# Kernel tuning notes

Measured on AMD Instinct MI355X. Metric: run time of the kernel, lower is better.

Reference implementation:

```python
import jax, jax.numpy as jnp
import numpy as np

V, E, SH, H = 10004, 300, 1024, 512
B, T = 128, 50
PAD = 10003


def setup_inputs() -> dict:
    key = jax.random.key(0)
    ks = jax.random.split(key, 13)
    s = 0.05
    emb = s * jax.random.normal(ks[0], (V, E), dtype=jnp.float32)
    emb = emb.at[PAD].set(0.0)  # padding_idx row is zero
    G = 2 * H  # GRU hidden size is 2*hid_size
    Wih = s * jax.random.normal(ks[1], (3 * G, E), dtype=jnp.float32)
    Whh = s * jax.random.normal(ks[2], (3 * G, G), dtype=jnp.float32)
    bih = s * jax.random.normal(ks[3], (3 * G,), dtype=jnp.float32)
    bhh = s * jax.random.normal(ks[4], (3 * G,), dtype=jnp.float32)
    W1 = s * jax.random.normal(ks[5], (H, SH), dtype=jnp.float32)
    b1 = s * jax.random.normal(ks[6], (H,), dtype=jnp.float32)
    W2 = s * jax.random.normal(ks[7], (E, G), dtype=jnp.float32)
    b2 = s * jax.random.normal(ks[8], (E,), dtype=jnp.float32)
    Wout = s * jax.random.normal(ks[9], (V, E), dtype=jnp.float32)
    ses_encoding = jax.random.normal(ks[10], (1, B, SH), dtype=jnp.float32)
    x = jax.random.randint(ks[11], (B, T), 0, 10000)
    return {"ses_encoding": ses_encoding, "x": x, "emb": emb, "Wih": Wih,
            "Whh": Whh, "bih": bih, "bhh": bhh, "W1": W1, "b1": b1,
            "W2": W2, "b2": b2, "Wout": Wout}


def reference(ses_encoding, x, emb, Wih, Whh, bih, bhh, W1, b1, W2, b2, Wout):
    hid = W1.shape[0]            # hid_size
    G = Whh.shape[1]             # 2*hid_size (GRU hidden)
    # ses_encoding = tanh(lin1(ses_encoding)), then viewed to [1, B, hid]
    ses = jnp.tanh(jnp.einsum('lbs,hs->lbh', ses_encoding, W1) + b1)[0]  # [B, hid]
    emb_all = emb[x]             # [B, T, E] (dropout inactive at eval)

    def step(h, e_t):
        # GRU hidden input each step: concat(prev_half, ses) -> [B, 2*hid]
        Hfull = jnp.concatenate([h, ses], axis=-1)
        gx = e_t @ Wih.T + bih                      # [B, 3G]
        gh = Hfull @ Whh.T + bhh                    # [B, 3G]
        r = jax.nn.sigmoid(gx[:, :G] + gh[:, :G])
        z = jax.nn.sigmoid(gx[:, G:2 * G] + gh[:, G:2 * G])
        n = jnp.tanh(gx[:, 2 * G:] + r * gh[:, 2 * G:])
        hnew = (1.0 - z) * n + z * Hfull            # [B, 2*hid]
        o = hnew @ W2.T + b2 + e_t                  # lin2(hid_o) + residual emb
        logits = o @ Wout.T                         # [B, V]
        return hnew[:, :hid], logits

    _, logits = jax.lax.scan(step, ses, jnp.swapaxes(emb_all, 0, 1))
    return jnp.swapaxes(logits, 0, 1)               # [B, T, V]
```

## Files before the change

kernel.cpp:

```cpp
#include <hip/hip_runtime.h>


typedef __bf16 bf16x8 __attribute__((ext_vector_type(8)));
typedef float f32x4 __attribute__((ext_vector_type(4)));
typedef unsigned long long u64;

struct CvtAll {
    const float* src[7];
    int srows[7], scols[7], sstride[7], soff[7], drows[7], dcols[7];
    __bf16* dst[7];
    int blk0[8];
    const int* x; const float* emb; __bf16* embbf;
};

__global__ void cvt_all_kernel(CvtAll p) {
    int bid = blockIdx.x;
    if (bid >= p.blk0[7]) {
        int idx = (bid - p.blk0[7]) * 256 + threadIdx.x;
        if (idx >= 6400 * 320) return;
        int m = idx / 320, c = idx - m * 320;
        int t = m >> 7, b = m & 127;
        int tok = p.x[b * 50 + t];
        float v = (c < 300) ? p.emb[(size_t)tok * 300 + c] : 0.0f;
        p.embbf[idx] = (__bf16)v;
        return;
    }
    int s = 0;
    while (s < 6 && bid >= p.blk0[s + 1]) ++s;
    int idx = (bid - p.blk0[s]) * 256 + threadIdx.x;
    int dc = p.dcols[s];
    int r = idx / dc, c = idx - r * dc;
    if (r >= p.drows[s]) return;
    float v = 0.0f;
    if (r < p.srows[s] && c < p.scols[s])
        v = p.src[s][(size_t)r * p.sstride[s] + p.soff[s] + c];
    p.dst[s][(size_t)r * dc + c] = (__bf16)v;
}

struct GemmParams {
    const __bf16* A; int lda;
    const __bf16* B; int ldb; int Brows;
    int K;
    const float* bias;
    float* outF; int ldo; int Nstore;
    __bf16* outBf;
    const __bf16* res;
    const float* add2;
    int ld2; int add2lim;
};

template <int EPI>
__launch_bounds__(256, 2)
__global__ void gemm_bt(GemmParams p) {
    __shared__ __bf16 As[128][40];
    __shared__ __bf16 Bs[128][40];

    const int tid = threadIdx.x;
    const int lane = tid & 63;
    const int wid = tid >> 6;
    const int wr = wid >> 1, wc = wid & 1;
    const int m0 = blockIdx.x * 128, c0 = blockIdx.y * 128;
    const int lrow = lane & 15;
    const int kq = lane >> 4;

    f32x4 acc[4][4];
#pragma unroll
    for (int i = 0; i < 4; ++i)
#pragma unroll
        for (int j = 0; j < 4; ++j) acc[i][j] = (f32x4){0.f, 0.f, 0.f, 0.f};

    for (int kb = 0; kb < p.K; kb += 32) {
#pragma unroll
        for (int i = 0; i < 2; ++i) {
            int chunk = i * 256 + tid;
            int row = chunk >> 2;
            int cc = (chunk & 3) * 8;
            bf16x8 va = *reinterpret_cast<const bf16x8*>(
                p.A + (size_t)(m0 + row) * p.lda + kb + cc);
            *reinterpret_cast<bf16x8*>(&As[row][cc]) = va;
            bf16x8 vb;
#pragma unroll
            for (int q = 0; q < 8; ++q) vb[q] = (__bf16)0.0f;
            int grow = c0 + row;
            if (grow < p.Brows)
                vb = *reinterpret_cast<const bf16x8*>(
                    p.B + (size_t)grow * p.ldb + kb + cc);
            *reinterpret_cast<bf16x8*>(&Bs[row][cc]) = vb;
        }
        __syncthreads();

        bf16x8 af[4], bfr[4];
#pragma unroll
        for (int m = 0; m < 4; ++m)
            af[m] = *reinterpret_cast<const bf16x8*>(&As[wr * 64 + m * 16 + lrow][kq * 8]);
#pragma unroll
        for (int n = 0; n < 4; ++n)
            bfr[n] = *reinterpret_cast<const bf16x8*>(&Bs[wc * 64 + n * 16 + lrow][kq * 8]);
#pragma unroll
        for (int m = 0; m < 4; ++m)
#pragma unroll
            for (int n = 0; n < 4; ++n)
                acc[m][n] = __builtin_amdgcn_mfma_f32_16x16x32_bf16(
                    af[m], bfr[n], acc[m][n], 0, 0, 0);
        __syncthreads();
    }

#pragma unroll
    for (int m = 0; m < 4; ++m) {
#pragma unroll
        for (int n = 0; n < 4; ++n) {
#pragma unroll
            for (int i = 0; i < 4; ++i) {
                int r = m0 + wr * 64 + m * 16 + kq * 4 + i;
                int c = c0 + wc * 64 + n * 16 + lrow;
                float v = acc[m][n][i];
                if constexpr (EPI == 1) {
                    v = tanhf(v + p.bias[c]);
                    p.outBf[(size_t)r * p.ldo + c] = (__bf16)v;
                    p.outF[(size_t)c * 128 + r] = v;
                } else if constexpr (EPI == 2) {
                    int ro = (r & 127) * 50 + (r >> 7);
                    if (c < 300) {
                        v += p.bias[c] + (float)p.res[(size_t)r * 320 + c];
                        p.outBf[(size_t)ro * 320 + c] = (__bf16)v;
                    } else if (c < 320) {
                        p.outBf[(size_t)ro * 320 + c] = (__bf16)0.0f;
                    }
                } else if constexpr (EPI == 3) {
                    if (c < p.Nstore) p.outF[(size_t)r * p.ldo + c] = v;
                } else {
                    if (c < p.Brows) {
                        float v2 = v + p.bias[r];
                        if (p.add2 && r < p.add2lim)
                            v2 += p.add2[(size_t)r * 128 + (c & 127)];
                        p.outF[(size_t)(c >> 7) * p.ldo + (size_t)r * 128 + (c & 127)] = v2;
                    }
                }
            }
        }
    }
}

#define SCAN_NB 64
__launch_bounds__(256, 1)
__global__ void scan_kernel(const __bf16* __restrict__ Whh_a,
                            const float* __restrict__ gxT,
                            const float* __restrict__ ghcT,
                            const float* __restrict__ sesT,
                            u64* __restrict__ F,
                            unsigned* __restrict__ cnt) {
    __shared__ char smem[131072];
    char* Ws = smem;
    char* Hs = smem + 98304;
    const int tid = threadIdx.x;
    const int lane = tid & 63;
    const int wid = tid >> 6;
    const int wr = wid >> 1, wc = wid & 1;
    const int bid = blockIdx.x;
    const int q = bid >> 4;
    const int j0 = (bid & 15) * 32;
    const int lrow = lane & 15, kq = lane >> 4;

    for (int it = 0; it < 24; ++it) {
        int c = it * 256 + tid;
        int rl = c >> 6, o16 = c & 63;
        int g = rl >> 5, jj = rl & 31;
        bf16x8 v = *reinterpret_cast<const bf16x8*>(
            Whh_a + (size_t)(g * 1024 + j0 + jj) * 512 + o16 * 8);
        *reinterpret_cast<bf16x8*>(Ws + rl * 1024 + ((o16 * 16) ^ ((rl & 7) << 4))) = v;
    }

    const int b_g = q * 32 + wc * 16 + lrow;
    const int jbase = j0 + wr * 16 + kq * 4;

    float cn[4], hprev[4], gcur[12], gpre[12];
#pragma unroll
    for (int i = 0; i < 4; ++i) {
        cn[i] = ghcT[(size_t)(2048 + jbase + i) * 128 + b_g];
        hprev[i] = sesT[(size_t)(jbase + i) * 128 + b_g];
    }
#pragma unroll
    for (int i = 0; i < 4; ++i) {
        gpre[i]     = gxT[(size_t)(jbase + i) * 128 + b_g];
        gpre[4 + i] = gxT[(size_t)(1024 + jbase + i) * 128 + b_g];
        gpre[8 + i] = gxT[(size_t)(2048 + jbase + i) * 128 + b_g];
    }

    for (int t = 0; t < 50; ++t) {
        for (int it = 0; it < 16; ++it) {
            int c = it * 256 + tid;
            int rl = c >> 7, o8 = c & 127;
            u64 v = __hip_atomic_load(
                F + ((size_t)t * 128 + q * 32 + rl) * 256 + o8,
                __ATOMIC_RELAXED, __HIP_MEMORY_SCOPE_AGENT);
            *reinterpret_cast<u64*>(Hs + rl * 1024 + ((o8 * 8) ^ ((rl & 7) << 4))) = v;
        }
#pragma unroll
        for (int i = 0; i < 12; ++i) gcur[i] = gpre[i];
        {
            int tn = (t < 49) ? t + 1 : 49;
            const float* gxt = gxT + (size_t)tn * 3072 * 128;
#pragma unroll
            for (int i = 0; i < 4; ++i) {
                gpre[i]     = gxt[(size_t)(jbase + i) * 128 + b_g];
                gpre[4 + i] = gxt[(size_t)(1024 + jbase + i) * 128 + b_g];
                gpre[8 + i] = gxt[(size_t)(2048 + jbase + i) * 128 + b_g];
            }
        }
        __syncthreads();

        f32x4 acc[3];
#pragma unroll
        for (int g = 0; g < 3; ++g) acc[g] = (f32x4){0.f, 0.f, 0.f, 0.f};
        const int hrow = wc * 16 + lrow;
        const int arow0 = wr * 16 + lrow;
        for (int kb = 0; kb < 16; ++kb) {
            int ko = kb * 64 + kq * 16;
            bf16x8 hfrag = *reinterpret_cast<const bf16x8*>(
                Hs + hrow * 1024 + (ko ^ ((hrow & 7) << 4)));
#pragma unroll
            for (int g = 0; g < 3; ++g) {
                int arow = g * 32 + arow0;
                bf16x8 wfrag = *reinterpret_cast<const bf16x8*>(
                    Ws + arow * 1024 + (ko ^ ((arow & 7) << 4)));
                acc[g] = __builtin_amdgcn_mfma_f32_16x16x32_bf16(
                    wfrag, hfrag, acc[g], 0, 0, 0);
            }
        }

        union { u64 u; __bf16 h[4]; } pk;
#pragma unroll
        for (int i = 0; i < 4; ++i) {
            float r = 1.0f / (1.0f + expf(-(gcur[i] + acc[0][i])));
            float z = 1.0f / (1.0f + expf(-(gcur[4 + i] + acc[1][i])));
            float nn = tanhf(gcur[8 + i] + r * (acc[2][i] + cn[i]));
            float hn = (1.0f - z) * nn + z * hprev[i];
            hprev[i] = hn;
            pk.h[i] = (__bf16)hn;
        }
        __hip_atomic_store(
            F + ((size_t)(t + 1) * 128 + b_g) * 256 + (jbase >> 2), pk.u,
            __ATOMIC_RELAXED, __HIP_MEMORY_SCOPE_AGENT);

        if (t < 49) {
            __syncthreads();
            if (tid == 0) {
                __hip_atomic_fetch_add(cnt + q * 32, 1u,
                                       __ATOMIC_RELAXED, __HIP_MEMORY_SCOPE_AGENT);
                unsigned tgt = (unsigned)(t + 1) * 16u;
                while (__hip_atomic_load(cnt + q * 32, __ATOMIC_RELAXED,
                                         __HIP_MEMORY_SCOPE_AGENT) < tgt)
                    __builtin_amdgcn_s_sleep(1);
            }
            __syncthreads();
        }
    }
}

__launch_bounds__(256, 1)
__global__ void tail_kernel(const __bf16* __restrict__ Whh_a,
                            const float* __restrict__ gxT,
                            const float* __restrict__ ghcT,
                            const float* __restrict__ sesT,
                            __bf16* __restrict__ F) {
    __shared__ char smem[131072];
    char* Ws = smem;
    char* Hs = smem + 98304;
    const int tid = threadIdx.x;
    const int lane = tid & 63;
    const int wid = tid >> 6;
    const int wr = wid >> 1, wc = wid & 1;
    const int bid = blockIdx.x;
    const int tseg = bid >> 6;
    const int rem = bid & 63;
    const int q = rem >> 4;
    const int j0 = 512 + (rem & 15) * 32;
    const int lrow = lane & 15, kq = lane >> 4;

    const int t0 = (tseg < 2) ? tseg * 13 : 26 + (tseg - 2) * 12;
    const int t1 = (tseg < 2) ? t0 + 13 : t0 + 12;

    for (int it = 0; it < 24; ++it) {
        int c = it * 256 + tid;
        int rl = c >> 6, o16 = c & 63;
        int g = rl >> 5, jj = rl & 31;
        bf16x8 v = *reinterpret_cast<const bf16x8*>(
            Whh_a + (size_t)(g * 1024 + j0 + jj) * 512 + o16 * 8);
        *reinterpret_cast<bf16x8*>(Ws + rl * 1024 + ((o16 * 16) ^ ((rl & 7) << 4))) = v;
    }

    const int b_g = q * 32 + wc * 16 + lrow;
    const int jbase = j0 + wr * 16 + kq * 4;

    float cn[4], sv[4];
#pragma unroll
    for (int i = 0; i < 4; ++i) {
        cn[i] = ghcT[(size_t)(2048 + jbase + i) * 128 + b_g];
        sv[i] = sesT[(size_t)(jbase + i - 512) * 128 + b_g];
    }

    for (int tt = t0; tt < t1; ++tt) {
        for (int it = 0; it < 8; ++it) {
            int c = it * 256 + tid;
            int rl = c >> 6, o16 = c & 63;
            bf16x8 v = *reinterpret_cast<const bf16x8*>(
                F + ((size_t)tt * 128 + q * 32 + rl) * 1024 + o16 * 8);
            *reinterpret_cast<bf16x8*>(Hs + rl * 1024 + ((o16 * 16) ^ ((rl & 7) << 4))) = v;
        }
        const float* gxt = gxT + (size_t)tt * 3072 * 128;
        float g0[12];
#pragma unroll
        for (int i = 0; i < 4; ++i) {
            g0[i]     = gxt[(size_t)(jbase + i) * 128 + b_g];
            g0[4 + i] = gxt[(size_t)(1024 + jbase + i) * 128 + b_g];
            g0[8 + i] = gxt[(size_t)(2048 + jbase + i) * 128 + b_g];
        }
        __syncthreads();

        f32x4 acc[3];
#pragma unroll
        for (int g = 0; g < 3; ++g) acc[g] = (f32x4){0.f, 0.f, 0.f, 0.f};
        const int hrow = wc * 16 + lrow;
        const int arow0 = wr * 16 + lrow;
        for (int kb = 0; kb < 16; ++kb) {
            int ko = kb * 64 + kq * 16;
            bf16x8 hfrag = *reinterpret_cast<const bf16x8*>(
                Hs + hrow * 1024 + (ko ^ ((hrow & 7) << 4)));
#pragma unroll
            for (int g = 0; g < 3; ++g) {
                int arow = g * 32 + arow0;
                bf16x8 wfrag = *reinterpret_cast<const bf16x8*>(
                    Ws + arow * 1024 + (ko ^ ((arow & 7) << 4)));
                acc[g] = __builtin_amdgcn_mfma_f32_16x16x32_bf16(
                    wfrag, hfrag, acc[g], 0, 0, 0);
            }
        }

        union { u64 u; __bf16 h[4]; } pk;
#pragma unroll
        for (int i = 0; i < 4; ++i) {
            float r = 1.0f / (1.0f + expf(-(g0[i] + acc[0][i])));
            float z = 1.0f / (1.0f + expf(-(g0[4 + i] + acc[1][i])));
            float nn = tanhf(g0[8 + i] + r * (acc[2][i] + cn[i]));
            pk.h[i] = (__bf16)((1.0f - z) * nn + z * sv[i]);
        }
        *reinterpret_cast<u64*>(F + ((size_t)(tt + 1) * 128 + b_g) * 1024 + jbase) = pk.u;
        __syncthreads();
    }
}

extern "C" void kernel_launch(void* const* d_in, const int* in_sizes, int n_in,
                              void* d_out, int out_size, void* d_ws, size_t ws_size,
                              hipStream_t stream) {
    const float* ses_enc = (const float*)d_in[0];
    const int*   x       = (const int*)d_in[1];
    const float* emb     = (const float*)d_in[2];
    const float* Wih     = (const float*)d_in[3];
    const float* Whh     = (const float*)d_in[4];
    const float* bih     = (const float*)d_in[5];
    const float* bhh     = (const float*)d_in[6];
    const float* W1      = (const float*)d_in[7];
    const float* b1      = (const float*)d_in[8];
    const float* W2      = (const float*)d_in[9];
    const float* b2      = (const float*)d_in[10];
    const float* Wout    = (const float*)d_in[11];
    float* out = (float*)d_out;

    char* ws = (char*)d_ws;
    float*  sesT      = (float*)(ws + 0);
    float*  ghcT      = (float*)(ws + 262144);
    __bf16* o_bf      = (__bf16*)(ws + 1835008);
    __bf16* W1_bf     = (__bf16*)(ws + 5931008);
    __bf16* Whh_a_bf  = (__bf16*)(ws + 6979584);
    __bf16* Whh_b_bf  = (__bf16*)(ws + 10125312);
    __bf16* Wih_bf    = (__bf16*)(ws + 13271040);
    __bf16* W2_bf     = (__bf16*)(ws + 15237120);
    __bf16* Wout_bf   = (__bf16*)(ws + 15851520);
    __bf16* sesenc_bf = (__bf16*)(ws + 22323200);
    unsigned* cnt     = (unsigned*)(ws + 22585344);

    char* ob = (char*)d_out;
    float*  gxT     = (float*)ob;
    __bf16* emb_bf  = (__bf16*)(ob + 80000000);
    __bf16* F       = (__bf16*)(ob + 88000000);

    dim3 blk(256);

    CvtAll ca;
    const float* csrc[7]  = {W1, Whh, Whh, Wih, W2, Wout, ses_enc};
    int csr[7]  = {512, 3072, 3072, 3072, 300, 10004, 128};
    int csc[7]  = {1024, 512, 512, 300, 1024, 300, 1024};
    int cst[7]  = {1024, 1024, 1024, 300, 1024, 300, 1024};
    int cso[7]  = {0, 0, 512, 0, 0, 0, 0};
    __bf16* cdst[7] = {W1_bf, Whh_a_bf, Whh_b_bf, Wih_bf, W2_bf, Wout_bf, sesenc_bf};
    int cdr[7]  = {512, 3072, 3072, 3072, 300, 10112, 128};
    int cdc[7]  = {1024, 512, 512, 320, 1024, 320, 1024};
    int b0 = 0;
    for (int s = 0; s < 7; ++s) {
        ca.src[s] = csrc[s]; ca.srows[s] = csr[s]; ca.scols[s] = csc[s];
        ca.sstride[s] = cst[s]; ca.soff[s] = cso[s];
        ca.dst[s] = cdst[s]; ca.drows[s] = cdr[s]; ca.dcols[s] = cdc[s];
        ca.blk0[s] = b0;
        b0 += (cdr[s] * cdc[s] + 255) / 256;
    }
    ca.blk0[7] = b0;
    ca.x = x; ca.emb = emb; ca.embbf = emb_bf;
    int total_blocks = b0 + (6400 * 320) / 256;
    cvt_all_kernel<<<total_blocks, 256, 0, stream>>>(ca);
    hipMemsetAsync(cnt, 0, 1024, stream);

    GemmParams P;

    P = {sesenc_bf, 1024, W1_bf, 1024, 512, 1024, b1, sesT, 1024, 512, F,
         nullptr, nullptr, 0, 0};
    gemm_bt<1><<<dim3(1, 4), blk, 0, stream>>>(P);

    P = {Whh_b_bf, 512, F, 1024, 128, 512, bhh, ghcT, 0, 0, nullptr,
         nullptr, nullptr, 0, 0};
    gemm_bt<4><<<dim3(24, 1), blk, 0, stream>>>(P);

    P = {Wih_bf, 320, emb_bf, 320, 6400, 320, bih, gxT, 3072 * 128, 0, nullptr,
         nullptr, ghcT, 0, 2048};
    gemm_bt<4><<<dim3(24, 50), blk, 0, stream>>>(P);

    scan_kernel<<<SCAN_NB, 256, 0, stream>>>(
        Whh_a_bf, gxT, ghcT, sesT, (u64*)F, cnt);

    tail_kernel<<<256, 256, 0, stream>>>(Whh_a_bf, gxT, ghcT, sesT, F);

    P = {F + 128 * 1024, 1024, W2_bf, 1024, 300, 1024, b2, nullptr, 0, 300, o_bf,
         emb_bf, nullptr, 0, 0};
    gemm_bt<2><<<dim3(50, 3), blk, 0, stream>>>(P);

    P = {o_bf, 320, Wout_bf, 320, 10112, 320, nullptr, out, 10004, 10004, nullptr,
         nullptr, nullptr, 0, 0};
    gemm_bt<3><<<dim3(50, 79), blk, 0, stream>>>(P);

    (void)in_sizes; (void)n_in; (void)out_size; (void)ws_size;
}
```

Before: 684.9 us.

## Prefetch next K tile into registers and widen GEMM K tile to 64

Restructures the bf16 MFMA GEMM main loop so that global loads for the next K block are issued into registers before the current block's MFMAs run. The staging into shared memory then happens at the top of the next iteration. The K tile doubles from 32 to 64, with shared arrays widened to match, which halves the number of barrier pairs per GEMM. This aims to hide global-memory latency behind compute, at the cost of more registers and LDS per block. It also assumes K is a multiple of 64.

```diff
diff --git a/kernel.cpp b/kernel.cpp
--- a/kernel.cpp
+++ b/kernel.cpp
@@ -52,8 +52,8 @@
 template <int EPI>
 __launch_bounds__(256, 2)
 __global__ void gemm_bt(GemmParams p) {
-    __shared__ __bf16 As[128][40];
-    __shared__ __bf16 Bs[128][40];
+    __shared__ __bf16 As[128][72];
+    __shared__ __bf16 Bs[128][72];
 
     const int tid = threadIdx.x;
     const int lane = tid & 63;
@@ -63,46 +63,79 @@
     const int lrow = lane & 15;
     const int kq = lane >> 4;
 
+    int srow[4], scol[4];
+#pragma unroll
+    for (int i = 0; i < 4; ++i) {
+        int chunk = i * 256 + tid;
+        srow[i] = chunk >> 3;
+        scol[i] = (chunk & 7) * 8;
+    }
+
     f32x4 acc[4][4];
 #pragma unroll
     for (int i = 0; i < 4; ++i)
 #pragma unroll
         for (int j = 0; j < 4; ++j) acc[i][j] = (f32x4){0.f, 0.f, 0.f, 0.f};
 
-    for (int kb = 0; kb < p.K; kb += 32) {
-#pragma unroll
-        for (int i = 0; i < 2; ++i) {
-            int chunk = i * 256 + tid;
-            int row = chunk >> 2;
-            int cc = (chunk & 3) * 8;
-            bf16x8 va = *reinterpret_cast<const bf16x8*>(
-                p.A + (size_t)(m0 + row) * p.lda + kb + cc);
-            *reinterpret_cast<bf16x8*>(&As[row][cc]) = va;
-            bf16x8 vb;
-#pragma unroll
-            for (int q = 0; q < 8; ++q) vb[q] = (__bf16)0.0f;
-            int grow = c0 + row;
-            if (grow < p.Brows)
-                vb = *reinterpret_cast<const bf16x8*>(
-                    p.B + (size_t)grow * p.ldb + kb + cc);
-            *reinterpret_cast<bf16x8*>(&Bs[row][cc]) = vb;
-        }
+    const int nkb = p.K >> 6;
+    bf16x8 ra[4], rb[4];
+#pragma unroll
+    for (int i = 0; i < 4; ++i) {
+        ra[i] = *reinterpret_cast<const bf16x8*>(
+            p.A + (size_t)(m0 + srow[i]) * p.lda + scol[i]);
+        bf16x8 z;
+#pragma unroll
+        for (int q = 0; q < 8; ++q) z[q] = (__bf16)0.0f;
+        int grow = c0 + srow[i];
+        rb[i] = (grow < p.Brows)
+            ? *reinterpret_cast<const bf16x8*>(p.B + (size_t)grow * p.ldb + scol[i])
+            : z;
+    }
+
+    for (int kb = 0; kb < nkb; ++kb) {
         __syncthreads();
-
-        bf16x8 af[4], bfr[4];
-#pragma unroll
-        for (int m = 0; m < 4; ++m)
-            af[m] = *reinterpret_cast<const bf16x8*>(&As[wr * 64 + m * 16 + lrow][kq * 8]);
-#pragma unroll
-        for (int n = 0; n < 4; ++n)
-            bfr[n] = *reinterpret_cast<const bf16x8*>(&Bs[wc * 64 + n * 16 + lrow][kq * 8]);
-#pragma unroll
-        for (int m = 0; m < 4; ++m)
+#pragma unroll
+        for (int i = 0; i < 4; ++i) {
+            *reinterpret_cast<bf16x8*>(&As[srow[i]][scol[i]]) = ra[i];
+            *reinterpret_cast<bf16x8*>(&Bs[srow[i]][scol[i]]) = rb[i];
+        }
+        __syncthreads();
+
+        if (kb + 1 < nkb) {
+            int ko = (kb + 1) << 6;
+#pragma unroll
+            for (int i = 0; i < 4; ++i) {
+                ra[i] = *reinterpret_cast<const bf16x8*>(
+                    p.A + (size_t)(m0 + srow[i]) * p.lda + ko + scol[i]);
+                bf16x8 z;
+#pragma unroll
+                for (int q = 0; q < 8; ++q) z[q] = (__bf16)0.0f;
+                int grow = c0 + srow[i];
+                rb[i] = (grow < p.Brows)
+                    ? *reinterpret_cast<const bf16x8*>(
+                          p.B + (size_t)grow * p.ldb + ko + scol[i])
+                    : z;
+            }
+        }
+
+#pragma unroll
+        for (int kk = 0; kk < 2; ++kk) {
+            bf16x8 af[4], bfr[4];
+#pragma unroll
+            for (int m = 0; m < 4; ++m)
+                af[m] = *reinterpret_cast<const bf16x8*>(
+                    &As[wr * 64 + m * 16 + lrow][kk * 32 + kq * 8]);
 #pragma unroll
             for (int n = 0; n < 4; ++n)
-                acc[m][n] = __builtin_amdgcn_mfma_f32_16x16x32_bf16(
-                    af[m], bfr[n], acc[m][n], 0, 0, 0);
-        __syncthreads();
+                bfr[n] = *reinterpret_cast<const bf16x8*>(
+                    &Bs[wc * 64 + n * 16 + lrow][kk * 32 + kq * 8]);
+#pragma unroll
+            for (int m = 0; m < 4; ++m)
+#pragma unroll
+                for (int n = 0; n < 4; ++n)
+                    acc[m][n] = __builtin_amdgcn_mfma_f32_16x16x32_bf16(
+                        af[m], bfr[n], acc[m][n], 0, 0, 0);
+        }
     }
 
 #pragma unroll
```

New measurement: 634.8 us. 1.08x faster.
